# Kernel optimization log

Measured on AMD Instinct MI355X. Metric: run time of the kernel, lower is better.

## Reference

```python
import jax, jax.numpy as jnp
import numpy as np

HIDDEN = 2048
HEADS = 16
HEAD_DIM = HIDDEN // HEADS
D_FF = 4 * HIDDEN
B, T = 2, 2048
LN_EPS = 1e-5


def setup_inputs() -> dict:
    key = jax.random.key(0)
    ks = jax.random.split(key, 12)
    s = 0.02
    x = jax.random.normal(ks[0], (B, T, HIDDEN), dtype=jnp.float32)
    # strict upper-triangular True == masked (causal)
    causal_mask = jnp.triu(jnp.ones((T, T), dtype=bool), k=1)
    # weights stored as [in, out] (equivalent to torch Linear weight.T)
    Wq = jax.random.normal(ks[1], (HIDDEN, HIDDEN), jnp.float32) * s
    Wk = jax.random.normal(ks[2], (HIDDEN, HIDDEN), jnp.float32) * s
    Wv = jax.random.normal(ks[3], (HIDDEN, HIDDEN), jnp.float32) * s
    Wo = jax.random.normal(ks[4], (HIDDEN, HIDDEN), jnp.float32) * s
    ln1_w = jnp.ones((HIDDEN,), jnp.float32)
    ln1_b = jnp.zeros((HIDDEN,), jnp.float32)
    ln2_w = jnp.ones((HIDDEN,), jnp.float32)
    ln2_b = jnp.zeros((HIDDEN,), jnp.float32)
    W1 = jax.random.normal(ks[5], (HIDDEN, D_FF), jnp.float32) * s
    b1 = jnp.zeros((D_FF,), jnp.float32)
    W2 = jax.random.normal(ks[6], (D_FF, HIDDEN), jnp.float32) * s
    b2 = jnp.zeros((HIDDEN,), jnp.float32)
    return dict(x=x, causal_mask=causal_mask, Wq=Wq, Wk=Wk, Wv=Wv, Wo=Wo,
                ln1_w=ln1_w, ln1_b=ln1_b, ln2_w=ln2_w, ln2_b=ln2_b,
                W1=W1, b1=b1, W2=W2, b2=b2)


def _layernorm(x, w, b):
    mu = jnp.mean(x, axis=-1, keepdims=True)
    var = jnp.mean(jnp.square(x - mu), axis=-1, keepdims=True)
    return (x - mu) * jax.lax.rsqrt(var + LN_EPS) * w + b


def reference(x, causal_mask, Wq, Wk, Wv, Wo, ln1_w, ln1_b, ln2_w, ln2_b, W1, b1, W2, b2):
    Bx, Tx, H = x.shape
    h = _layernorm(x, ln1_w, ln1_b)
    # [B, T, heads, head_dim] -> [B, heads, T, head_dim]
    q = (h @ Wq).reshape(Bx, Tx, HEADS, HEAD_DIM).transpose(0, 2, 1, 3)
    k = (h @ Wk).reshape(Bx, Tx, HEADS, HEAD_DIM).transpose(0, 2, 1, 3)
    v = (h @ Wv).reshape(Bx, Tx, HEADS, HEAD_DIM).transpose(0, 2, 1, 3)
    scale = 1.0 / jnp.sqrt(jnp.float32(HEAD_DIM))
    scores = jnp.einsum('bhqd,bhkd->bhqk', q, k) * scale  # [B, heads, T, T]
    scores = jnp.where(causal_mask, -jnp.inf, scores)
    attn = jax.nn.softmax(scores, axis=-1)
    out = jnp.einsum('bhqk,bhkd->bhqd', attn, v)  # [B, heads, T, head_dim]
    out = out.transpose(0, 2, 1, 3).reshape(Bx, Tx, H)
    x = x + out @ Wo
    h2 = _layernorm(x, ln2_w, ln2_b)
    mlp = jax.nn.silu(h2 @ W1 + b1) @ W2 + b2
    return x + mlp
```

## Files before the change

kernel.cpp:

```cpp
#include <hip/hip_runtime.h>

#define HID 2048
#define NH 16
#define DH 128
#define DFF 8192
#define BB 2
#define TT 2048
#define MROWS 4096

typedef __bf16 bf16x8 __attribute__((ext_vector_type(8)));
typedef __bf16 bf16x4 __attribute__((ext_vector_type(4)));
typedef float  f32x4  __attribute__((ext_vector_type(4)));

__device__ __forceinline__ f32x4 mfma16(bf16x8 a, bf16x8 b, f32x4 c) {
    return __builtin_amdgcn_mfma_f32_16x16x32_bf16(a, b, c, 0, 0, 0);
}

__device__ __forceinline__ void gload_lds16(const __bf16* gsrc, __bf16* ldst) {
    __builtin_amdgcn_global_load_lds(
        (const __attribute__((address_space(1))) void*)gsrc,
        (__attribute__((address_space(3))) void*)ldst, 16, 0, 0);
}

template<int K, int N>
__global__ __launch_bounds__(256) void transpose_bf16_kernel(
    const float* __restrict__ W, __bf16* __restrict__ Wt) {
    __shared__ float tile[64][65];
    int tx = threadIdx.x;
    int ty = threadIdx.y;
    int n0 = blockIdx.x * 64;
    int k0 = blockIdx.y * 64;
    #pragma unroll
    for (int i = 0; i < 16; i++) {
        int kk = ty * 16 + i;
        tile[tx][kk] = W[(size_t)(k0 + kk) * N + n0 + tx];
    }
    __syncthreads();
    #pragma unroll
    for (int i = 0; i < 16; i++) {
        int nn = ty * 16 + i;
        Wt[(size_t)(n0 + nn) * K + k0 + tx] = (__bf16)tile[nn][tx];
    }
}

__global__ __launch_bounds__(256) void ln_kernel(
    const float* __restrict__ x, const float* __restrict__ gw,
    const float* __restrict__ gb, __bf16* __restrict__ out) {
    int row = blockIdx.x;
    int t = threadIdx.x;
    const float* xr = x + (size_t)row * HID;
    float4 v0 = *(const float4*)(xr + t * 8);
    float4 v1 = *(const float4*)(xr + t * 8 + 4);
    float xv[8] = {v0.x, v0.y, v0.z, v0.w, v1.x, v1.y, v1.z, v1.w};
    float s = 0.f, q = 0.f;
    #pragma unroll
    for (int j = 0; j < 8; j++) { s += xv[j]; q += xv[j] * xv[j]; }
    #pragma unroll
    for (int off = 1; off < 64; off <<= 1) {
        s += __shfl_xor(s, off);
        q += __shfl_xor(q, off);
    }
    __shared__ float ssum[4], ssq[4];
    if ((t & 63) == 0) { ssum[t >> 6] = s; ssq[t >> 6] = q; }
    __syncthreads();
    s = ssum[0] + ssum[1] + ssum[2] + ssum[3];
    q = ssq[0] + ssq[1] + ssq[2] + ssq[3];
    float mu = s * (1.0f / HID);
    float var = q * (1.0f / HID) - mu * mu;
    float rs = rsqrtf(var + 1e-5f);
    bf16x8 o;
    #pragma unroll
    for (int j = 0; j < 8; j++)
        o[j] = (__bf16)((xv[j] - mu) * rs * gw[t * 8 + j] + gb[t * 8 + j]);
    *(bf16x8*)(out + (size_t)row * HID + t * 8) = o;
}

__global__ __launch_bounds__(256) void init_out_kernel(
    const float* __restrict__ x1, const float* __restrict__ b2,
    float* __restrict__ out) {
    int i = blockIdx.x * 256 + threadIdx.x;
    float4 a = ((const float4*)x1)[i];
    float4 bb = ((const float4*)b2)[i & (HID / 4 - 1)];
    float4 o = {a.x + bb.x, a.y + bb.y, a.z + bb.z, a.w + bb.w};
    ((float4*)out)[i] = o;
}

template<int EPI, int KSPLIT, int N, int K>
__global__ __launch_bounds__(512, 2) void gemm256(
    const __bf16* __restrict__ A, const __bf16* __restrict__ Bt,
    void* __restrict__ C0, void* __restrict__ C1, void* __restrict__ C2,
    const float* __restrict__ resid, const float* __restrict__ bias, int nN) {
    constexpr int BK = 64;
    constexpr int KS = K / KSPLIT;
    constexpr int NT = KS / BK;

    __shared__ __align__(16) __bf16 As[2][16384];
    __shared__ __align__(16) __bf16 Bs[2][16384];

    int tid = threadIdx.x;
    int w = tid >> 6, l = tid & 63;
    int wm = w >> 2, wn = w & 3;
    int qi = l & 15, g = l >> 4;

    int nwg = gridDim.x;
    int bid = blockIdx.x;
    int wg = (bid & 7) * (nwg >> 3) + (bid >> 3);
    int nMN = nwg / KSPLIT;
    int tileid = wg % nMN;
    int kh = wg / nMN;
    int bm = tileid / nN, bn = tileid % nN;
    int row0 = bm * 256, col0 = bn * 256;
    int kb0 = kh * KS;

    int offA[2][2], offB[2][2];
    #pragma unroll
    for (int h = 0; h < 2; h++)
        #pragma unroll
        for (int i = 0; i < 2; i++) {
            int slot = i * 512 + tid;
            int r = slot >> 3, u8 = slot & 7;
            offA[h][i] = (row0 + h * 128 + r) * K + kb0 + (u8 ^ (r & 7)) * 8;
            offB[h][i] = (col0 + h * 128 + r) * K + kb0 + (u8 ^ (r & 7)) * 8;
        }
    int dstoff = w * 512;

    f32x4 acc[8][4] = {};
    bf16x8 aF[4][2], bF0[2][2], bF1[2][2];

    auto stageA = [&](int u, int h) {
        #pragma unroll
        for (int i = 0; i < 2; i++)
            gload_lds16(A + offA[h][i] + u * BK,
                        &As[u & 1][h * 8192 + i * 4096 + dstoff]);
    };
    auto stageB = [&](int u, int h) {
        #pragma unroll
        for (int i = 0; i < 2; i++)
            gload_lds16(Bt + offB[h][i] + u * BK,
                        &Bs[u & 1][h * 8192 + i * 4096 + dstoff]);
    };
    auto loadA = [&](int s, int qm) {
        #pragma unroll
        for (int mi = 0; mi < 4; mi++) {
            int rA = qm * 128 + wm * 64 + mi * 16 + qi;
            #pragma unroll
            for (int kk = 0; kk < 2; kk++) {
                int byt = rA * 128 + ((kk * 64 + g * 16) ^ ((rA & 7) << 4));
                aF[mi][kk] = *(const bf16x8*)((const char*)As[s] + byt);
            }
        }
    };
    auto loadB = [&](bf16x8 (&bF)[2][2], int s, int qn) {
        #pragma unroll
        for (int ni = 0; ni < 2; ni++) {
            int rB = qn * 128 + wn * 32 + ni * 16 + qi;
            #pragma unroll
            for (int kk = 0; kk < 2; kk++) {
                int byt = rB * 128 + ((kk * 64 + g * 16) ^ ((rB & 7) << 4));
                bF[ni][kk] = *(const bf16x8*)((const char*)Bs[s] + byt);
            }
        }
    };

    #define MMAC(BF, FMB, FNB)                                             \
        asm volatile("s_waitcnt lgkmcnt(0)" ::: "memory");                 \
        __builtin_amdgcn_sched_barrier(0);                                 \
        __builtin_amdgcn_s_setprio(1);                                     \
        _Pragma("unroll")                                                  \
        for (int kk = 0; kk < 2; kk++)                                     \
            _Pragma("unroll")                                              \
            for (int mi = 0; mi < 4; mi++)                                 \
                _Pragma("unroll")                                          \
                for (int ni = 0; ni < 2; ni++)                             \
                    acc[(FMB) + mi][(FNB) + ni] =                          \
                        mfma16(aF[mi][kk], BF[ni][kk],                     \
                               acc[(FMB) + mi][(FNB) + ni]);               \
        __builtin_amdgcn_s_setprio(0);

    stageA(0, 0); stageB(0, 0); stageA(0, 1); stageB(0, 1);
    if (NT > 1) { stageA(1, 0); stageB(1, 0); stageA(1, 1); }
    asm volatile("s_waitcnt vmcnt(6)" ::: "memory");
    __builtin_amdgcn_s_barrier();

    for (int t = 0; t < NT; t++) {
        int s = t & 1;
        loadA(s, 0); loadB(bF0, s, 0);
        if (t + 1 < NT) stageB(t + 1, 1);
        __builtin_amdgcn_s_barrier();
        MMAC(bF0, 0, 0)
        __builtin_amdgcn_s_barrier();
        loadB(bF1, s, 1);
        if (t + 2 < NT) stageA(t + 2, 0);
        __builtin_amdgcn_s_barrier();
        MMAC(bF1, 0, 2)
        __builtin_amdgcn_s_barrier();
        loadA(s, 1);
        if (t + 2 < NT) stageB(t + 2, 0);
        __builtin_amdgcn_s_barrier();
        MMAC(bF0, 4, 0)
        __builtin_amdgcn_s_barrier();
        if (t + 2 < NT) stageA(t + 2, 1);
        __builtin_amdgcn_s_barrier();
        MMAC(bF1, 4, 2)
        if (t + 2 < NT)      asm volatile("s_waitcnt vmcnt(6)" ::: "memory");
        else if (t + 1 < NT) asm volatile("s_waitcnt vmcnt(0)" ::: "memory");
        __builtin_amdgcn_s_barrier();
    }
    #undef MMAC

    #pragma unroll
    for (int fm = 0; fm < 8; fm++) {
        int qm = fm >> 2, mi = fm & 3;
        int Rb = row0 + qm * 128 + wm * 64 + mi * 16 + g * 4;
        #pragma unroll
        for (int fn = 0; fn < 4; fn++) {
            int qn = fn >> 1, ni = fn & 1;
            int C = col0 + qn * 128 + wn * 32 + ni * 16 + qi;
            f32x4 v = acc[fm][fn];
            if constexpr (EPI == 6) {
                int region = C >> 11;
                int Cl = C & 2047;
                if (region < 2) {
                    __bf16* dst = (__bf16*)(region == 0 ? C0 : C1);
                    #pragma unroll
                    for (int r = 0; r < 4; r++)
                        dst[(size_t)(Rb + r) * 2048 + Cl] = (__bf16)v[r];
                } else {
                    bf16x4 pk;
                    #pragma unroll
                    for (int r = 0; r < 4; r++) pk[r] = (__bf16)v[r];
                    int b = Rb >> 11, t0 = Rb & 2047, hh = Cl >> 7, d = Cl & 127;
                    *(bf16x4*)((__bf16*)C2 +
                        ((size_t)(b * NH + hh) * DH + d) * TT + t0) = pk;
                }
            } else {
                #pragma unroll
                for (int r = 0; r < 4; r++) {
                    size_t idx = (size_t)(Rb + r) * N + C;
                    if constexpr (EPI == 2) {
                        ((float*)C0)[idx] = resid[idx] + v[r];
                    } else if constexpr (EPI == 3) {
                        float u = v[r] + bias[C];
                        ((__bf16*)C0)[idx] = (__bf16)(u / (1.f + __expf(-u)));
                    } else if constexpr (EPI == 5) {
                        atomicAdd((float*)C0 + idx, v[r]);
                    }
                }
            }
        }
    }
}

__global__ __launch_bounds__(256) void attn_kernel(
    const __bf16* __restrict__ qh, const __bf16* __restrict__ kh,
    const __bf16* __restrict__ vt, __bf16* __restrict__ out) {
    __shared__ __align__(16) __bf16 Ks[64 * 128];
    __shared__ __align__(16) __bf16 Vts[128 * 64];
    __shared__ __align__(16) __bf16 plds[4][1024];
    int tid = threadIdx.x;
    int w = tid >> 6, l = tid & 63;
    int qi = l & 15, g = l >> 4;
    int bh = blockIdx.y;
    int b = bh >> 4, hd = bh & 15;
    int qtile = gridDim.x - 1 - blockIdx.x;
    int qbase = qtile * 64 + w * 16;
    int qg = qbase + qi;

    const __bf16* qrow = qh + ((size_t)b * TT + qg) * HID + hd * DH;
    const __bf16* kbase = kh + (size_t)b * TT * HID + hd * DH;
    const __bf16* vtb = vt + (size_t)bh * DH * TT;

    bf16x8 bq[4];
    #pragma unroll
    for (int kc = 0; kc < 4; kc++)
        bq[kc] = *(const bf16x8*)(qrow + kc * 32 + g * 8);

    f32x4 O[8] = {};
    float m_run = -3.0e38f, l_run = 0.f;
    const float scale = 0.08838834764831845f;
    int nt = qtile + 1;

    for (int it = 0; it < nt; it++) {
        int kv0 = it * 64;
        __syncthreads();
        #pragma unroll
        for (int i = 0; i < 4; i++) {
            int j = (w * 4 + i) * 64 + l;
            int r = j >> 4, u = j & 15;
            int cb = (u * 16) ^ ((r & 7) << 4);
            gload_lds16(kbase + (size_t)(kv0 + r) * HID + (cb >> 1),
                        Ks + (w * 4 + i) * 512);
        }
        #pragma unroll
        for (int i = 0; i < 4; i++) {
            int j = (w * 4 + i) * 64 + l;
            int r = j >> 3, u = j & 7;
            int cb = (u * 16) ^ ((r & 7) << 4);
            gload_lds16(vtb + (size_t)r * TT + kv0 + (cb >> 1),
                        Vts + (w * 4 + i) * 512);
        }
        __syncthreads();

        f32x4 st[4] = {};
        #pragma unroll
        for (int t = 0; t < 4; t++) {
            #pragma unroll
            for (int kc = 0; kc < 4; kc++) {
                int row = t * 16 + qi;
                int cb = (kc * 64 + g * 16) ^ ((qi & 7) << 4);
                bf16x8 ak = *(const bf16x8*)(Ks + row * 128 + (cb >> 1));
                st[t] = mfma16(ak, bq[kc], st[t]);
            }
        }
        float s[16];
        #pragma unroll
        for (int t = 0; t < 4; t++)
            #pragma unroll
            for (int r = 0; r < 4; r++) s[t * 4 + r] = st[t][r] * scale;
        #pragma unroll
        for (int i = 0; i < 16; i++) {
            int kvg = kv0 + (i >> 2) * 16 + g * 4 + (i & 3);
            if (kvg > qg) s[i] = -3.0e38f;
        }
        float mt = s[0];
        #pragma unroll
        for (int i = 1; i < 16; i++) mt = fmaxf(mt, s[i]);
        mt = fmaxf(mt, __shfl_xor(mt, 16));
        mt = fmaxf(mt, __shfl_xor(mt, 32));
        float m_new = fmaxf(m_run, mt);
        float alpha = __expf(m_run - m_new);
        float p[16], ps = 0.f;
        #pragma unroll
        for (int i = 0; i < 16; i++) { p[i] = __expf(s[i] - m_new); ps += p[i]; }
        ps += __shfl_xor(ps, 16);
        ps += __shfl_xor(ps, 32);
        l_run = l_run * alpha + ps;
        m_run = m_new;

        #pragma unroll
        for (int t = 0; t < 4; t++) {
            bf16x4 pk;
            #pragma unroll
            for (int r = 0; r < 4; r++) pk[r] = (__bf16)p[t * 4 + r];
            int cb = (t * 32 + g * 8) ^ ((qi & 7) << 4);
            *(bf16x4*)(&plds[w][qi * 64 + (cb >> 1)]) = pk;
        }

        float av[4];
        #pragma unroll
        for (int r = 0; r < 4; r++) av[r] = __shfl(alpha, (g << 4) | (g * 4 + r));
        #pragma unroll
        for (int oc = 0; oc < 8; oc++)
            #pragma unroll
            for (int r = 0; r < 4; r++) O[oc][r] *= av[r];

        #pragma unroll
        for (int h = 0; h < 2; h++) {
            int cbp = (h * 64 + g * 16) ^ ((qi & 7) << 4);
            bf16x8 ap = *(const bf16x8*)(&plds[w][qi * 64 + (cbp >> 1)]);
            #pragma unroll
            for (int oc = 0; oc < 8; oc++) {
                int row = oc * 16 + qi;
                int cb = (h * 64 + g * 16) ^ ((qi & 7) << 4);
                bf16x8 bv = *(const bf16x8*)(Vts + row * 64 + (cb >> 1));
                O[oc] = mfma16(ap, bv, O[oc]);
            }
        }
    }

    float linv[4];
    #pragma unroll
    for (int r = 0; r < 4; r++) {
        float lq = __shfl(l_run, (g << 4) | (g * 4 + r));
        linv[r] = 1.0f / lq;
    }
    __bf16* op = out + ((size_t)b * TT + qbase) * HID + hd * DH;
    #pragma unroll
    for (int oc = 0; oc < 8; oc++)
        #pragma unroll
        for (int r = 0; r < 4; r++)
            op[(size_t)(g * 4 + r) * HID + oc * 16 + qi] = (__bf16)(O[oc][r] * linv[r]);
}

extern "C" void kernel_launch(void* const* d_in, const int* in_sizes, int n_in,
                              void* d_out, int out_size, void* d_ws, size_t ws_size,
                              hipStream_t stream) {
    const float* x    = (const float*)d_in[0];
    const float* Wq   = (const float*)d_in[2];
    const float* Wk   = (const float*)d_in[3];
    const float* Wv   = (const float*)d_in[4];
    const float* Wo   = (const float*)d_in[5];
    const float* ln1w = (const float*)d_in[6];
    const float* ln1b = (const float*)d_in[7];
    const float* ln2w = (const float*)d_in[8];
    const float* ln2b = (const float*)d_in[9];
    const float* W1   = (const float*)d_in[10];
    const float* b1   = (const float*)d_in[11];
    const float* W2   = (const float*)d_in[12];
    const float* b2   = (const float*)d_in[13];
    float* outp = (float*)d_out;

    char* ws = (char*)d_ws;
    const size_t SZ_W   = (size_t)HID * HID * 2;
    const size_t SZ_WF  = (size_t)HID * DFF * 2;
    const size_t SZ_ACT = (size_t)MROWS * HID * 2;
    const size_t SZ_X32 = (size_t)MROWS * HID * 4;

    __bf16* wqT  = (__bf16*)(ws);
    __bf16* wkT  = (__bf16*)(ws + SZ_W);
    __bf16* wvT  = (__bf16*)(ws + 2 * SZ_W);
    __bf16* woT  = (__bf16*)(ws + 3 * SZ_W);
    __bf16* w1T  = (__bf16*)(ws + 4 * SZ_W);
    __bf16* w2T  = (__bf16*)(ws + 4 * SZ_W + SZ_WF);
    __bf16* h    = (__bf16*)(ws + 4 * SZ_W + 2 * SZ_WF);
    float*  x1   = (float*) (ws + 4 * SZ_W + 2 * SZ_WF + SZ_ACT);
    char*   base = ws + 4 * SZ_W + 2 * SZ_WF + SZ_ACT + SZ_X32;
    __bf16* qb   = (__bf16*)(base);
    __bf16* kb   = (__bf16*)(base + SZ_ACT);
    __bf16* vtb  = (__bf16*)(base + 2 * SZ_ACT);
    __bf16* attn = (__bf16*)(base + 3 * SZ_ACT);
    __bf16* mlp1 = (__bf16*)(base);

    dim3 blk256(256), blk512(512);
    transpose_bf16_kernel<HID, HID><<<dim3(32, 32), dim3(64, 4), 0, stream>>>(Wq, wqT);
    transpose_bf16_kernel<HID, HID><<<dim3(32, 32), dim3(64, 4), 0, stream>>>(Wk, wkT);
    transpose_bf16_kernel<HID, HID><<<dim3(32, 32), dim3(64, 4), 0, stream>>>(Wv, wvT);
    transpose_bf16_kernel<HID, HID><<<dim3(32, 32), dim3(64, 4), 0, stream>>>(Wo, woT);
    transpose_bf16_kernel<HID, DFF><<<dim3(128, 32), dim3(64, 4), 0, stream>>>(W1, w1T);
    transpose_bf16_kernel<DFF, HID><<<dim3(32, 128), dim3(64, 4), 0, stream>>>(W2, w2T);

    ln_kernel<<<MROWS, blk256, 0, stream>>>(x, ln1w, ln1b, h);

    gemm256<6, 1, 6144, HID><<<384, blk512, 0, stream>>>(
        h, wqT, qb, kb, vtb, nullptr, nullptr, 24);

    attn_kernel<<<dim3(TT / 64, BB * NH), blk256, 0, stream>>>(qb, kb, vtb, attn);

    gemm256<2, 1, HID, HID><<<128, blk512, 0, stream>>>(
        attn, woT, x1, nullptr, nullptr, x, nullptr, 8);

    ln_kernel<<<MROWS, blk256, 0, stream>>>(x1, ln2w, ln2b, h);

    gemm256<3, 1, DFF, HID><<<512, blk512, 0, stream>>>(
        h, w1T, mlp1, nullptr, nullptr, nullptr, b1, 32);

    init_out_kernel<<<MROWS * HID / 4 / 256, blk256, 0, stream>>>(x1, b2, outp);
    gemm256<5, 2, HID, DFF><<<256, blk512, 0, stream>>>(
        mlp1, w2T, outp, nullptr, nullptr, nullptr, nullptr, 8);
}
```

Baseline: 788.5 us.

## Split-K the Wo projection, precompute LDS fragment offsets, relax launch bounds

The Wo projection GEMM now uses split-K=2 with atomic accumulation (EPI 5) into an x1 buffer pre-initialised with the residual x. This doubles the grid from 128 to 256 workgroups so more CUs are busy. The LDS fragment loads now use precomputed base pointers and XOR offsets instead of per-load index arithmetic. Launch bounds drop from 2 to 1 workgroups per CU, giving the compiler more registers at the possible cost of occupancy. The extra init kernel and the atomics add memory traffic, and the atomics make the summation order nondeterministic.

```diff
diff --git a/kernel.cpp b/kernel.cpp
--- a/kernel.cpp
+++ b/kernel.cpp
@@ -75,18 +75,21 @@
     *(bf16x8*)(out + (size_t)row * HID + t * 8) = o;
 }
 
-__global__ __launch_bounds__(256) void init_out_kernel(
-    const float* __restrict__ x1, const float* __restrict__ b2,
+template<int HB>
+__global__ __launch_bounds__(256) void init_resid_kernel(
+    const float* __restrict__ src, const float* __restrict__ bias,
     float* __restrict__ out) {
     int i = blockIdx.x * 256 + threadIdx.x;
-    float4 a = ((const float4*)x1)[i];
-    float4 bb = ((const float4*)b2)[i & (HID / 4 - 1)];
-    float4 o = {a.x + bb.x, a.y + bb.y, a.z + bb.z, a.w + bb.w};
-    ((float4*)out)[i] = o;
+    float4 a = ((const float4*)src)[i];
+    if constexpr (HB) {
+        float4 bb = ((const float4*)bias)[i & (HID / 4 - 1)];
+        a.x += bb.x; a.y += bb.y; a.z += bb.z; a.w += bb.w;
+    }
+    ((float4*)out)[i] = a;
 }
 
 template<int EPI, int KSPLIT, int N, int K>
-__global__ __launch_bounds__(512, 2) void gemm256(
+__global__ __launch_bounds__(512, 1) void gemm256(
     const __bf16* __restrict__ A, const __bf16* __restrict__ Bt,
     void* __restrict__ C0, void* __restrict__ C1, void* __restrict__ C2,
     const float* __restrict__ resid, const float* __restrict__ bias, int nN) {
@@ -124,6 +127,11 @@
         }
     int dstoff = w * 512;
 
+    int xk0 = (g * 16) ^ ((qi & 7) << 4);
+    int xk1 = (64 + g * 16) ^ ((qi & 7) << 4);
+    int aoff = wm * 8192 + qi * 128;
+    int boff = wn * 4096 + qi * 128;
+
     f32x4 acc[8][4] = {};
     bf16x8 aF[4][2], bF0[2][2], bF1[2][2];
 
@@ -140,25 +148,21 @@
                         &Bs[u & 1][h * 8192 + i * 4096 + dstoff]);
     };
     auto loadA = [&](int s, int qm) {
+        const char* pa0 = (const char*)As[s] + aoff + xk0;
+        const char* pa1 = (const char*)As[s] + aoff + xk1;
         #pragma unroll
         for (int mi = 0; mi < 4; mi++) {
-            int rA = qm * 128 + wm * 64 + mi * 16 + qi;
-            #pragma unroll
-            for (int kk = 0; kk < 2; kk++) {
-                int byt = rA * 128 + ((kk * 64 + g * 16) ^ ((rA & 7) << 4));
-                aF[mi][kk] = *(const bf16x8*)((const char*)As[s] + byt);
-            }
+            aF[mi][0] = *(const bf16x8*)(pa0 + qm * 16384 + mi * 2048);
+            aF[mi][1] = *(const bf16x8*)(pa1 + qm * 16384 + mi * 2048);
         }
     };
     auto loadB = [&](bf16x8 (&bF)[2][2], int s, int qn) {
+        const char* pb0 = (const char*)Bs[s] + boff + xk0;
+        const char* pb1 = (const char*)Bs[s] + boff + xk1;
         #pragma unroll
         for (int ni = 0; ni < 2; ni++) {
-            int rB = qn * 128 + wn * 32 + ni * 16 + qi;
-            #pragma unroll
-            for (int kk = 0; kk < 2; kk++) {
-                int byt = rB * 128 + ((kk * 64 + g * 16) ^ ((rB & 7) << 4));
-                bF[ni][kk] = *(const bf16x8*)((const char*)Bs[s] + byt);
-            }
+            bF[ni][0] = *(const bf16x8*)(pb0 + qn * 16384 + ni * 2048);
+            bF[ni][1] = *(const bf16x8*)(pb1 + qn * 16384 + ni * 2048);
         }
     };
 
@@ -436,15 +440,16 @@
 
     attn_kernel<<<dim3(TT / 64, BB * NH), blk256, 0, stream>>>(qb, kb, vtb, attn);
 
-    gemm256<2, 1, HID, HID><<<128, blk512, 0, stream>>>(
-        attn, woT, x1, nullptr, nullptr, x, nullptr, 8);
+    init_resid_kernel<0><<<MROWS * HID / 4 / 256, blk256, 0, stream>>>(x, nullptr, x1);
+    gemm256<5, 2, HID, HID><<<256, blk512, 0, stream>>>(
+        attn, woT, x1, nullptr, nullptr, nullptr, nullptr, 8);
 
     ln_kernel<<<MROWS, blk256, 0, stream>>>(x1, ln2w, ln2b, h);
 
     gemm256<3, 1, DFF, HID><<<512, blk512, 0, stream>>>(
         h, w1T, mlp1, nullptr, nullptr, nullptr, b1, 32);
 
-    init_out_kernel<<<MROWS * HID / 4 / 256, blk256, 0, stream>>>(x1, b2, outp);
+    init_resid_kernel<1><<<MROWS * HID / 4 / 256, blk256, 0, stream>>>(x1, b2, outp);
     gemm256<5, 2, HID, DFF><<<256, blk512, 0, stream>>>(
         mlp1, w2T, outp, nullptr, nullptr, nullptr, nullptr, 8);
 }
```

Measured after the change: 793.1 us. No clear change (+0.6%).
